# Kernel tuning notes

Measured on AMD Instinct MI355X. Metric: run time of the kernel, lower is better.

Reference implementation:

```python
import jax, jax.numpy as jnp
import numpy as np

DIM = 512
GLBL = 108
N = 100000
NUM_SEGMENTS = 1024


def setup_inputs() -> dict:
    key = jax.random.key(0)
    ks = jax.random.split(key, 9)
    x = jax.random.normal(ks[0], (N, DIM), dtype=jnp.float32)
    glbl_x = jax.random.normal(ks[1], (N, GLBL), dtype=jnp.float32)
    batch = jnp.sort(jax.random.randint(ks[2], (N,), 0, NUM_SEGMENTS, dtype=jnp.int32))
    # MLP params: (dim+108 -> dim), (dim -> dim), (dim -> 1)
    s0 = 1.0 / np.sqrt(DIM + GLBL)
    s1 = 1.0 / np.sqrt(DIM)
    W0 = jax.random.uniform(ks[3], (DIM + GLBL, DIM), jnp.float32, -s0, s0)
    b0 = jax.random.uniform(ks[4], (DIM,), jnp.float32, -s0, s0)
    W1 = jax.random.uniform(ks[5], (DIM, DIM), jnp.float32, -s1, s1)
    b1 = jax.random.uniform(ks[6], (DIM,), jnp.float32, -s1, s1)
    W2 = jax.random.uniform(ks[7], (DIM, 1), jnp.float32, -s1, s1)
    b2 = jax.random.uniform(ks[8], (1,), jnp.float32, -s1, s1)
    return {"x": x, "batch": batch, "glbl_x": glbl_x,
            "W0": W0, "b0": b0, "W1": W1, "b1": b1, "W2": W2, "b2": b2}


def segment_softmax(logits, seg, num_segments):
    # logits: [N, 1]; per-segment numerically-stable softmax (torch_geometric softmax)
    m = jax.ops.segment_max(logits, seg, num_segments=num_segments)  # [G, 1]
    e = jnp.exp(logits - m[seg])
    s = jax.ops.segment_sum(e, seg, num_segments=num_segments)       # [G, 1]
    return e / (s[seg] + 1e-16)


def reference(x, batch, glbl_x, W0, b0, W1, b1, W2, b2):
    out = jnp.concatenate([x, glbl_x], axis=-1)          # [N, dim+108]
    out = jax.nn.softplus(out @ W0 + b0)                 # [N, dim]
    out = jax.nn.softplus(out @ W1 + b1)                 # [N, dim]
    out = out @ W2 + b2                                  # [N, 1]
    return segment_softmax(out, batch, NUM_SEGMENTS)     # [N, 1]
```

## Files before the change

kernel.cpp:

```cpp
#include <hip/hip_runtime.h>
#include <hip/hip_bf16.h>
#include <math.h>


#define NSEG 1024

typedef __attribute__((ext_vector_type(8))) short short8;
typedef __attribute__((ext_vector_type(4))) float f32x4;

__device__ __forceinline__ unsigned short f2bf(float f) {
  __hip_bfloat16 h = __float2bfloat16(f);
  return *reinterpret_cast<unsigned short*>(&h);
}
__device__ __forceinline__ float softplus_fast(float z) {
  float t = __expf(-fabsf(z));
  return fmaxf(z, 0.f) + __logf(1.f + t);
}
__device__ __forceinline__ void gll16(const unsigned short* g, unsigned short* l) {
  __builtin_amdgcn_global_load_lds(
      (const __attribute__((address_space(1))) void*)g,
      (__attribute__((address_space(3))) void*)l, 16, 0, 0);
}
__device__ __forceinline__ int xcd_swz(int bid, int nwg) {
  int q = nwg >> 3, r = nwg & 7, x = bid & 7, i = bid >> 3;
  return (x < r ? x * (q + 1) : r * (q + 1) + (x - r) * q) + i;
}

__global__ __launch_bounds__(256) void prep(const float* __restrict__ W0,
                                            const float* __restrict__ W1,
                                            unsigned short* __restrict__ W0T,
                                            unsigned short* __restrict__ W1T,
                                            float* __restrict__ logits, int Mp) {
  int t = blockIdx.x * 256 + threadIdx.x;
  if (t < 512 * 640) {
    int n = t / 640, k = t % 640;
    W0T[t] = f2bf(k < 620 ? W0[(size_t)k * 512 + n] : 0.f);
    return;
  }
  t -= 512 * 640;
  if (t < 512 * 512) {
    int n = t / 512, k = t % 512;
    W1T[t] = f2bf(W1[(size_t)k * 512 + n]);
    return;
  }
  t -= 512 * 512;
  if (t < Mp) logits[t] = 0.f;
}

__global__ __launch_bounds__(256) void pack(const float* __restrict__ x,
                                            const float* __restrict__ gx,
                                            unsigned short* __restrict__ X16,
                                            unsigned short* __restrict__ G16,
                                            int N, int Mp) {
  int t = blockIdx.x * 256 + threadIdx.x;
  union { unsigned short u[8]; uint4 q; } v;
  if (t < Mp * 64) {
    int row = t >> 6, c = t & 63;
    if (row >= N) {
#pragma unroll
      for (int j = 0; j < 8; ++j) v.u[j] = 0;
    } else {
      const float4* p = (const float4*)(x + (size_t)row * 512 + c * 8);
      float4 a = p[0], b = p[1];
      v.u[0] = f2bf(a.x); v.u[1] = f2bf(a.y); v.u[2] = f2bf(a.z); v.u[3] = f2bf(a.w);
      v.u[4] = f2bf(b.x); v.u[5] = f2bf(b.y); v.u[6] = f2bf(b.z); v.u[7] = f2bf(b.w);
    }
    *reinterpret_cast<uint4*>(X16 + (size_t)row * 512 + c * 8) = v.q;
    return;
  }
  t -= Mp * 64;
  if (t < Mp * 16) {
    int row = t >> 4, c = t & 15;
#pragma unroll
    for (int j = 0; j < 8; ++j) {
      int col = c * 8 + j;
      v.u[j] = (row < N && col < 108) ? f2bf(gx[(size_t)row * 108 + col]) : 0;
    }
    *reinterpret_cast<uint4*>(G16 + (size_t)row * 128 + c * 8) = v.q;
  }
}

template <int K, bool SPLITA, bool FUSE>
__global__ __launch_bounds__(256, 2) void gemm_bf16(const unsigned short* __restrict__ A1,
                                                    const unsigned short* __restrict__ A2,
                                                    const unsigned short* __restrict__ WT,
                                                    const float* __restrict__ bias,
                                                    unsigned short* __restrict__ C,
                                                    const float* __restrict__ W2,
                                                    float* __restrict__ logits, int nwg) {
  constexpr int KT = K / 32;
  __shared__ unsigned short As[2][256 * 32];
  __shared__ unsigned short Ws[2][128 * 32];
  const int L = xcd_swz(blockIdx.x, nwg);
  const int nt = L & 3, mt = L >> 2;
  const int tid = threadIdx.x, lane = tid & 63, wid = tid >> 6;
  const int wm = wid >> 1, wn = wid & 1;
  const int lm = lane & 15, rch = lane >> 4;

  const unsigned short* Ag = A1 + (size_t)(mt * 256) * 512;
  const unsigned short* A2g = SPLITA ? A2 + (size_t)(mt * 256) * 128 : nullptr;
  const unsigned short* Wg = WT + (size_t)(nt * 128) * K;

  f32x4 acc[8][4] = {};

  auto stage = [&](int buf, int kb) {
#pragma unroll
    for (int i2 = 0; i2 < 4; ++i2) {
      int f = i2 * 256 + tid;
      int row = f >> 2;
      int sc = ((f & 3) ^ ((row >> 1) & 3)) << 3;
      if constexpr (SPLITA) {
        if (kb < 512) gll16(Ag + (size_t)row * 512 + kb + sc, &As[buf][f * 8]);
        else          gll16(A2g + (size_t)row * 128 + (kb - 512) + sc, &As[buf][f * 8]);
      } else {
        gll16(Ag + (size_t)row * 512 + kb + sc, &As[buf][f * 8]);
      }
    }
#pragma unroll
    for (int i2 = 0; i2 < 2; ++i2) {
      int f = i2 * 256 + tid;
      int row = f >> 2;
      int sc = ((f & 3) ^ ((row >> 1) & 3)) << 3;
      gll16(Wg + (size_t)row * K + kb + sc, &Ws[buf][f * 8]);
    }
  };

  stage(0, 0);

  for (int kt = 0; kt < KT; ++kt) {
    const int cur = kt & 1;
    __syncthreads();
    if (kt + 1 < KT) stage(cur ^ 1, (kt + 1) * 32);

    short8 af[8], wf[4];
#pragma unroll
    for (int mi = 0; mi < 8; ++mi) {
      int rw = wm * 128 + mi * 16 + lm;
      af[mi] = *reinterpret_cast<const short8*>(
          &As[cur][rw * 32 + ((rch ^ ((rw >> 1) & 3)) << 3)]);
    }
#pragma unroll
    for (int ni = 0; ni < 4; ++ni) {
      int rw = wn * 64 + ni * 16 + lm;
      wf[ni] = *reinterpret_cast<const short8*>(
          &Ws[cur][rw * 32 + ((rch ^ ((rw >> 1) & 3)) << 3)]);
    }
    __builtin_amdgcn_s_setprio(1);
#pragma unroll
    for (int mi = 0; mi < 8; ++mi)
#pragma unroll
      for (int ni = 0; ni < 4; ++ni)
        acc[mi][ni] = __builtin_amdgcn_mfma_f32_16x16x32_bf16(wf[ni], af[mi], acc[mi][ni], 0, 0, 0);
    __builtin_amdgcn_s_setprio(0);
  }

#pragma unroll
  for (int mi = 0; mi < 8; ++mi) {
    const int m = mt * 256 + wm * 128 + mi * 16 + lm;
    float part = 0.f;
#pragma unroll
    for (int ni = 0; ni < 4; ++ni) {
      const int n0 = nt * 128 + wn * 64 + ni * 16 + (rch << 2);
      const f32x4 bb = *reinterpret_cast<const f32x4*>(bias + n0);
      f32x4 v = acc[mi][ni];
      if constexpr (!FUSE) {
        union { unsigned short u[4]; uint2 qv; } o;
#pragma unroll
        for (int rr = 0; rr < 4; ++rr) o.u[rr] = f2bf(softplus_fast(v[rr] + bb[rr]));
        *reinterpret_cast<uint2*>(C + (size_t)m * 512 + n0) = o.qv;
      } else {
        const f32x4 wv = *reinterpret_cast<const f32x4*>(W2 + n0);
#pragma unroll
        for (int rr = 0; rr < 4; ++rr) part += softplus_fast(v[rr] + bb[rr]) * wv[rr];
      }
    }
    if constexpr (FUSE) {
      part += __shfl_xor(part, 16);
      part += __shfl_xor(part, 32);
      if (lane < 16) atomicAdd(logits + m, part);
    }
  }
}

__global__ __launch_bounds__(256) void segsoftmax(const float* __restrict__ logits,
                                                  const int* __restrict__ batch,
                                                  float* __restrict__ out, int N) {
  const int g = blockIdx.x;
  const int tid = threadIdx.x;
  int lo = 0, hi = N;
  while (lo < hi) { int mid = (lo + hi) >> 1; if (batch[mid] < g) lo = mid + 1; else hi = mid; }
  const int beg = lo;
  hi = N;
  while (lo < hi) { int mid = (lo + hi) >> 1; if (batch[mid] < g + 1) lo = mid + 1; else hi = mid; }
  const int end = lo;
  if (beg >= end) return;

  __shared__ float sh[4];
  float m = -INFINITY;
  for (int i = beg + tid; i < end; i += 256) m = fmaxf(m, logits[i]);
#pragma unroll
  for (int o = 32; o; o >>= 1) m = fmaxf(m, __shfl_down(m, o));
  if ((tid & 63) == 0) sh[tid >> 6] = m;
  __syncthreads();
  m = fmaxf(fmaxf(sh[0], sh[1]), fmaxf(sh[2], sh[3]));
  __syncthreads();

  float s = 0.f;
  for (int i = beg + tid; i < end; i += 256) s += expf(logits[i] - m);
#pragma unroll
  for (int o = 32; o; o >>= 1) s += __shfl_down(s, o);
  if ((tid & 63) == 0) sh[tid >> 6] = s;
  __syncthreads();
  s = sh[0] + sh[1] + sh[2] + sh[3];

  const float inv = 1.f / (s + 1e-16f);
  for (int i = beg + tid; i < end; i += 256) out[i] = expf(logits[i] - m) * inv;
}

extern "C" void kernel_launch(void* const* d_in, const int* in_sizes, int n_in,
                              void* d_out, int out_size, void* d_ws, size_t ws_size,
                              hipStream_t stream) {
  const float* x = (const float*)d_in[0];
  const int* batch = (const int*)d_in[1];
  const float* gx = (const float*)d_in[2];
  const float* W0 = (const float*)d_in[3];
  const float* b0 = (const float*)d_in[4];
  const float* W1 = (const float*)d_in[5];
  const float* b1 = (const float*)d_in[6];
  const float* W2 = (const float*)d_in[7];
  float* out = (float*)d_out;

  const int N = in_sizes[1];
  const int Mp = ((N + 255) / 256) * 256;
  const int nwg = (Mp / 256) * 4;

  auto align256 = [](size_t v) { return (v + 255) & ~(size_t)255; };
  char* ws = (char*)d_ws;
  size_t off = 0;
  unsigned short* X16 = (unsigned short*)(ws + off); off = align256(off + (size_t)Mp * 512 * 2);
  unsigned short* G16 = (unsigned short*)(ws + off); off = align256(off + (size_t)Mp * 128 * 2);
  unsigned short* W0T = (unsigned short*)(ws + off); off = align256(off + (size_t)512 * 640 * 2);
  unsigned short* W1T = (unsigned short*)(ws + off); off = align256(off + (size_t)512 * 512 * 2);
  unsigned short* H0 = (unsigned short*)(ws + off);  off = align256(off + (size_t)Mp * 512 * 2);
  float* logits = (float*)(ws + off);                off = align256(off + (size_t)Mp * 4);
  (void)ws_size; (void)n_in; (void)out_size;

  const int prep_elems = 512 * 640 + 512 * 512 + Mp;
  prep<<<(prep_elems + 255) / 256, 256, 0, stream>>>(W0, W1, W0T, W1T, logits, Mp);
  pack<<<(Mp * 80 + 255) / 256, 256, 0, stream>>>(x, gx, X16, G16, N, Mp);

  gemm_bf16<640, true, false><<<nwg, 256, 0, stream>>>(X16, G16, W0T, b0, H0, nullptr, nullptr, nwg);
  gemm_bf16<512, false, true><<<nwg, 256, 0, stream>>>(H0, nullptr, W1T, b1, nullptr, W2, logits, nwg);

  segsoftmax<<<NSEG, 256, 0, stream>>>(logits, batch, out, N);
}
```

Before: 327.5 us.

## Use 8-wave 256x256 GEMM tiles with 4-slot pipelined LDS staging

Replaces the 256-thread 256x128 GEMM with a 512-thread kernel computing 256x256 tiles. It uses a 4-slot LDS ring that stages two k-tiles ahead, and interleaves staging, barriers and MFMA quarters with explicit vmcnt/lgkmcnt waits. The pack kernel becomes grid-stride with a fixed 2048 blocks and also takes over zeroing logits from prep. The larger tile halves redundant A loads, but it uses much more LDS (128KB) and hand-tuned wait counts that risk occupancy and correctness fragility.

```diff
diff --git a/kernel.cpp b/kernel.cpp
--- a/kernel.cpp
+++ b/kernel.cpp
@@ -16,7 +16,7 @@
   float t = __expf(-fabsf(z));
   return fmaxf(z, 0.f) + __logf(1.f + t);
 }
-__device__ __forceinline__ void gll16(const unsigned short* g, unsigned short* l) {
+__device__ __forceinline__ void gll16(const void* g, void* l) {
   __builtin_amdgcn_global_load_lds(
       (const __attribute__((address_space(1))) void*)g,
       (__attribute__((address_space(3))) void*)l, 16, 0, 0);
@@ -29,8 +29,7 @@
 __global__ __launch_bounds__(256) void prep(const float* __restrict__ W0,
                                             const float* __restrict__ W1,
                                             unsigned short* __restrict__ W0T,
-                                            unsigned short* __restrict__ W1T,
-                                            float* __restrict__ logits, int Mp) {
+                                            unsigned short* __restrict__ W1T) {
   int t = blockIdx.x * 256 + threadIdx.x;
   if (t < 512 * 640) {
     int n = t / 640, k = t % 640;
@@ -41,117 +40,144 @@
   if (t < 512 * 512) {
     int n = t / 512, k = t % 512;
     W1T[t] = f2bf(W1[(size_t)k * 512 + n]);
-    return;
-  }
-  t -= 512 * 512;
-  if (t < Mp) logits[t] = 0.f;
+  }
 }
 
 __global__ __launch_bounds__(256) void pack(const float* __restrict__ x,
                                             const float* __restrict__ gx,
                                             unsigned short* __restrict__ X16,
                                             unsigned short* __restrict__ G16,
+                                            float* __restrict__ logits,
                                             int N, int Mp) {
-  int t = blockIdx.x * 256 + threadIdx.x;
-  union { unsigned short u[8]; uint4 q; } v;
-  if (t < Mp * 64) {
-    int row = t >> 6, c = t & 63;
-    if (row >= N) {
-#pragma unroll
-      for (int j = 0; j < 8; ++j) v.u[j] = 0;
+  const int total = Mp * 80 + (Mp >> 2);
+  for (int t = blockIdx.x * 256 + threadIdx.x; t < total; t += gridDim.x * 256) {
+    union { unsigned short u[8]; uint4 q; } v;
+    if (t < Mp * 64) {
+      int row = t >> 6, c = t & 63;
+      if (row >= N) {
+#pragma unroll
+        for (int j = 0; j < 8; ++j) v.u[j] = 0;
+      } else {
+        const float4* p = (const float4*)(x + (size_t)row * 512 + c * 8);
+        float4 a = p[0], b = p[1];
+        v.u[0] = f2bf(a.x); v.u[1] = f2bf(a.y); v.u[2] = f2bf(a.z); v.u[3] = f2bf(a.w);
+        v.u[4] = f2bf(b.x); v.u[5] = f2bf(b.y); v.u[6] = f2bf(b.z); v.u[7] = f2bf(b.w);
+      }
+      *reinterpret_cast<uint4*>(X16 + (size_t)row * 512 + c * 8) = v.q;
+    } else if (t < Mp * 80) {
+      int t2 = t - Mp * 64;
+      int row = t2 >> 4, c = t2 & 15;
+#pragma unroll
+      for (int j = 0; j < 8; ++j) {
+        int col = c * 8 + j;
+        v.u[j] = (row < N && col < 108) ? f2bf(gx[(size_t)row * 108 + col]) : 0;
+      }
+      *reinterpret_cast<uint4*>(G16 + (size_t)row * 128 + c * 8) = v.q;
     } else {
-      const float4* p = (const float4*)(x + (size_t)row * 512 + c * 8);
-      float4 a = p[0], b = p[1];
-      v.u[0] = f2bf(a.x); v.u[1] = f2bf(a.y); v.u[2] = f2bf(a.z); v.u[3] = f2bf(a.w);
-      v.u[4] = f2bf(b.x); v.u[5] = f2bf(b.y); v.u[6] = f2bf(b.z); v.u[7] = f2bf(b.w);
-    }
-    *reinterpret_cast<uint4*>(X16 + (size_t)row * 512 + c * 8) = v.q;
-    return;
-  }
-  t -= Mp * 64;
-  if (t < Mp * 16) {
-    int row = t >> 4, c = t & 15;
-#pragma unroll
-    for (int j = 0; j < 8; ++j) {
-      int col = c * 8 + j;
-      v.u[j] = (row < N && col < 108) ? f2bf(gx[(size_t)row * 108 + col]) : 0;
-    }
-    *reinterpret_cast<uint4*>(G16 + (size_t)row * 128 + c * 8) = v.q;
+      int i = (t - Mp * 80) << 2;
+      *reinterpret_cast<float4*>(logits + i) = float4{0.f, 0.f, 0.f, 0.f};
+    }
   }
 }
 
 template <int K, bool SPLITA, bool FUSE>
-__global__ __launch_bounds__(256, 2) void gemm_bf16(const unsigned short* __restrict__ A1,
-                                                    const unsigned short* __restrict__ A2,
-                                                    const unsigned short* __restrict__ WT,
-                                                    const float* __restrict__ bias,
-                                                    unsigned short* __restrict__ C,
-                                                    const float* __restrict__ W2,
-                                                    float* __restrict__ logits, int nwg) {
+__global__ __launch_bounds__(512, 2) void gemm8p(const unsigned short* __restrict__ A1,
+                                                 const unsigned short* __restrict__ A2,
+                                                 const unsigned short* __restrict__ WT,
+                                                 const float* __restrict__ bias,
+                                                 unsigned short* __restrict__ C,
+                                                 const float* __restrict__ W2,
+                                                 float* __restrict__ logits, int nwg) {
   constexpr int KT = K / 32;
-  __shared__ unsigned short As[2][256 * 32];
-  __shared__ unsigned short Ws[2][128 * 32];
+  __shared__ unsigned short Ab[4][2][128 * 32];
+  __shared__ unsigned short Bb[4][2][128 * 32];
   const int L = xcd_swz(blockIdx.x, nwg);
-  const int nt = L & 3, mt = L >> 2;
+  const int nt = L & 1, mt = L >> 1;
   const int tid = threadIdx.x, lane = tid & 63, wid = tid >> 6;
-  const int wm = wid >> 1, wn = wid & 1;
+  const int wm = wid >> 2, wn = wid & 3, bh = wn >> 1;
   const int lm = lane & 15, rch = lane >> 4;
-
-  const unsigned short* Ag = A1 + (size_t)(mt * 256) * 512;
-  const unsigned short* A2g = SPLITA ? A2 + (size_t)(mt * 256) * 128 : nullptr;
-  const unsigned short* Wg = WT + (size_t)(nt * 128) * K;
+  const int wrow = (wn & 1) * 64;
+
+  const int sr = tid >> 2, scs = tid & 3;
+  const int sch = (scs ^ ((sr >> 1) & 3)) << 3;
 
   f32x4 acc[8][4] = {};
 
-  auto stage = [&](int buf, int kb) {
-#pragma unroll
-    for (int i2 = 0; i2 < 4; ++i2) {
-      int f = i2 * 256 + tid;
-      int row = f >> 2;
-      int sc = ((f & 3) ^ ((row >> 1) & 3)) << 3;
+  auto stage_half = [&](int slot, int ktile, int h) {
+    const int k = ktile * 32 + sch;
+    if (h < 2) {
+      const int row = mt * 256 + h * 128 + sr;
+      const unsigned short* src;
       if constexpr (SPLITA) {
-        if (kb < 512) gll16(Ag + (size_t)row * 512 + kb + sc, &As[buf][f * 8]);
-        else          gll16(A2g + (size_t)row * 128 + (kb - 512) + sc, &As[buf][f * 8]);
+        src = (k < 512) ? A1 + (size_t)row * 512 + k
+                        : A2 + (size_t)row * 128 + (k - 512);
       } else {
-        gll16(Ag + (size_t)row * 512 + kb + sc, &As[buf][f * 8]);
-      }
-    }
-#pragma unroll
-    for (int i2 = 0; i2 < 2; ++i2) {
-      int f = i2 * 256 + tid;
-      int row = f >> 2;
-      int sc = ((f & 3) ^ ((row >> 1) & 3)) << 3;
-      gll16(Wg + (size_t)row * K + kb + sc, &Ws[buf][f * 8]);
-    }
-  };
-
-  stage(0, 0);
+        src = A1 + (size_t)row * 512 + k;
+      }
+      gll16(src, &Ab[slot][h][tid * 8]);
+    } else {
+      const int row = nt * 256 + (h - 2) * 128 + sr;
+      gll16(WT + (size_t)row * K + k, &Bb[slot][h - 2][tid * 8]);
+    }
+  };
+
+  short8 af[4], wf[2];
+  auto read_af = [&](int slot, int mibase) {
+#pragma unroll
+    for (int i = 0; i < 4; ++i) {
+      int rw = (mibase + i) * 16 + lm;
+      af[i] = *reinterpret_cast<const short8*>(
+          &Ab[slot][wm][rw * 32 + ((rch ^ ((rw >> 1) & 3)) << 3)]);
+    }
+  };
+  auto read_wf = [&](int slot, int nibase) {
+#pragma unroll
+    for (int i = 0; i < 2; ++i) {
+      int rw = wrow + (nibase + i) * 16 + lm;
+      wf[i] = *reinterpret_cast<const short8*>(
+          &Bb[slot][bh][rw * 32 + ((rch ^ ((rw >> 1) & 3)) << 3)]);
+    }
+  };
+  auto mfma8 = [&](int mibase, int nibase) {
+    asm volatile("s_waitcnt lgkmcnt(0)" ::: "memory");
+    __builtin_amdgcn_sched_barrier(0);
+    __builtin_amdgcn_s_setprio(1);
+#pragma unroll
+    for (int i = 0; i < 4; ++i)
+#pragma unroll
+      for (int j = 0; j < 2; ++j)
+        acc[mibase + i][nibase + j] = __builtin_amdgcn_mfma_f32_16x16x32_bf16(
+            wf[j], af[i], acc[mibase + i][nibase + j], 0, 0, 0);
+    __builtin_amdgcn_s_setprio(0);
+  };
+
+#pragma unroll
+  for (int h = 0; h < 4; ++h) stage_half(0, 0, h);
+#pragma unroll
+  for (int h = 0; h < 4; ++h) stage_half(1, 1, h);
 
   for (int kt = 0; kt < KT; ++kt) {
-    const int cur = kt & 1;
-    __syncthreads();
-    if (kt + 1 < KT) stage(cur ^ 1, (kt + 1) * 32);
-
-    short8 af[8], wf[4];
-#pragma unroll
-    for (int mi = 0; mi < 8; ++mi) {
-      int rw = wm * 128 + mi * 16 + lm;
-      af[mi] = *reinterpret_cast<const short8*>(
-          &As[cur][rw * 32 + ((rch ^ ((rw >> 1) & 3)) << 3)]);
-    }
-#pragma unroll
-    for (int ni = 0; ni < 4; ++ni) {
-      int rw = wn * 64 + ni * 16 + lm;
-      wf[ni] = *reinterpret_cast<const short8*>(
-          &Ws[cur][rw * 32 + ((rch ^ ((rw >> 1) & 3)) << 3)]);
-    }
-    __builtin_amdgcn_s_setprio(1);
-#pragma unroll
-    for (int mi = 0; mi < 8; ++mi)
-#pragma unroll
-      for (int ni = 0; ni < 4; ++ni)
-        acc[mi][ni] = __builtin_amdgcn_mfma_f32_16x16x32_bf16(wf[ni], af[mi], acc[mi][ni], 0, 0, 0);
-    __builtin_amdgcn_s_setprio(0);
+    const int slot = kt & 3, sst = (kt + 2) & 3;
+    const bool st = (kt + 2) < KT;
+    if (kt < KT - 2) asm volatile("s_waitcnt vmcnt(4)" ::: "memory");
+    else             asm volatile("s_waitcnt vmcnt(0)" ::: "memory");
+    if (st) stage_half(sst, kt + 2, 0);
+    __builtin_amdgcn_s_barrier();
+    read_af(slot, 0);
+    read_wf(slot, 0);
+    mfma8(0, 0);
+    if (st) stage_half(sst, kt + 2, 1);
+    __builtin_amdgcn_s_barrier();
+    read_wf(slot, 2);
+    mfma8(0, 2);
+    if (st) stage_half(sst, kt + 2, 2);
+    __builtin_amdgcn_s_barrier();
+    read_af(slot, 4);
+    mfma8(4, 2);
+    if (st) stage_half(sst, kt + 2, 3);
+    __builtin_amdgcn_s_barrier();
+    read_wf(slot, 0);
+    mfma8(4, 0);
   }
 
 #pragma unroll
@@ -160,7 +186,7 @@
     float part = 0.f;
 #pragma unroll
     for (int ni = 0; ni < 4; ++ni) {
-      const int n0 = nt * 128 + wn * 64 + ni * 16 + (rch << 2);
+      const int n0 = nt * 256 + wn * 64 + ni * 16 + (rch << 2);
       const f32x4 bb = *reinterpret_cast<const f32x4*>(bias + n0);
       f32x4 v = acc[mi][ni];
       if constexpr (!FUSE) {
@@ -232,7 +258,7 @@
 
   const int N = in_sizes[1];
   const int Mp = ((N + 255) / 256) * 256;
-  const int nwg = (Mp / 256) * 4;
+  const int nwg = (Mp / 256) * 2;
 
   auto align256 = [](size_t v) { return (v + 255) & ~(size_t)255; };
   char* ws = (char*)d_ws;
@@ -245,12 +271,14 @@
   float* logits = (float*)(ws + off);                off = align256(off + (size_t)Mp * 4);
   (void)ws_size; (void)n_in; (void)out_size;
 
-  const int prep_elems = 512 * 640 + 512 * 512 + Mp;
-  prep<<<(prep_elems + 255) / 256, 256, 0, stream>>>(W0, W1, W0T, W1T, logits, Mp);
-  pack<<<(Mp * 80 + 255) / 256, 256, 0, stream>>>(x, gx, X16, G16, N, Mp);
-
-  gemm_bf16<640, true, false><<<nwg, 256, 0, stream>>>(X16, G16, W0T, b0, H0, nullptr, nullptr, nwg);
-  gemm_bf16<512, false, true><<<nwg, 256, 0, stream>>>(H0, nullptr, W1T, b1, nullptr, W2, logits, nwg);
+  const int prep_elems = 512 * 640 + 512 * 512;
+  prep<<<(prep_elems + 255) / 256, 256, 0, stream>>>(W0, W1, W0T, W1T);
+  pack<<<2048, 256, 0, stream>>>(x, gx, X16, G16, logits, N, Mp);
+
+  gemm8p<640, true, false><<<nwg, 512, 0, stream>>>(X16, G16, W0T, b0, H0,
+                                                    nullptr, nullptr, nwg);
+  gemm8p<512, false, true><<<nwg, 512, 0, stream>>>(H0, nullptr, W1T, b1,
+                                                    nullptr, W2, logits, nwg);
 
   segsoftmax<<<NSEG, 256, 0, stream>>>(logits, batch, out, N);
 }
```

Result: slower. 389.9 us (+19.0%).
